# Kernel optimization log

Hardware: AMD Instinct MI355X
Metric: run time of the kernel (lower is better)

## Reference

```python
import jax, jax.numpy as jnp
import numpy as np

POOLED_H, POOLED_W = 7, 7
SPATIAL_SCALE = 0.25
SAMPLING_RATIO = 2
ALIGNED = True

N_IMG, C, H, W = 4, 256, 200, 200
N_ROIS = 1024
IMG_SIZE = H / SPATIAL_SCALE  # 800.0, image-space extent


def setup_inputs() -> dict:
    key = jax.random.key(0)
    k_in, k_b, k_c, k_s = jax.random.split(key, 4)
    inp = jax.random.normal(k_in, (N_IMG, C, H, W), dtype=jnp.float32)
    # Boxes in image coordinates (xyxy), first column = batch index.
    b = jax.random.randint(k_b, (N_ROIS,), 0, N_IMG).astype(jnp.float32)
    ctr = jax.random.uniform(k_c, (N_ROIS, 2), minval=0.0, maxval=IMG_SIZE)
    sz = jax.random.uniform(k_s, (N_ROIS, 2), minval=16.0, maxval=320.0)
    x1 = jnp.clip(ctr[:, 0] - sz[:, 0] * 0.5, 0.0, IMG_SIZE)
    y1 = jnp.clip(ctr[:, 1] - sz[:, 1] * 0.5, 0.0, IMG_SIZE)
    x2 = jnp.clip(ctr[:, 0] + sz[:, 0] * 0.5, 0.0, IMG_SIZE)
    y2 = jnp.clip(ctr[:, 1] + sz[:, 1] * 0.5, 0.0, IMG_SIZE)
    rois = jnp.stack([b, x1, y1, x2, y2], axis=1)
    return {"input": inp, "rois": rois}


def _roi_align(feat_nchw, rois):
    """Faithful port of torchvision.ops.roi_align (avg mode, aligned=True)."""
    n, c, h, w = feat_nchw.shape
    ph, pw, sr = POOLED_H, POOLED_W, SAMPLING_RATIO
    offset = 0.5 if ALIGNED else 0.0

    b_idx = rois[:, 0].astype(jnp.int32)                      # [R]
    x1 = rois[:, 1] * SPATIAL_SCALE - offset
    y1 = rois[:, 2] * SPATIAL_SCALE - offset
    x2 = rois[:, 3] * SPATIAL_SCALE - offset
    y2 = rois[:, 4] * SPATIAL_SCALE - offset
    roi_w, roi_h = x2 - x1, y2 - y1
    if not ALIGNED:
        roi_w = jnp.maximum(roi_w, 1.0)
        roi_h = jnp.maximum(roi_h, 1.0)
    bin_h = roi_h / ph                                        # [R]
    bin_w = roi_w / pw

    # Sample-point grid: per output bin, sr x sr interior points.
    frac = (jnp.arange(sr, dtype=jnp.float32) + 0.5) / sr     # [sr]
    # y coords: [R, ph, sr], x coords: [R, pw, sr]
    ys = y1[:, None, None] + (jnp.arange(ph, dtype=jnp.float32)[None, :, None] + frac[None, None, :]) * bin_h[:, None, None]
    xs = x1[:, None, None] + (jnp.arange(pw, dtype=jnp.float32)[None, :, None] + frac[None, None, :]) * bin_w[:, None, None]
    # Broadcast to full grid [R, ph, pw, sr, sr]
    y = ys[:, :, None, :, None] * jnp.ones((1, 1, pw, 1, sr), jnp.float32)
    x = xs[:, None, :, None, :] * jnp.ones((1, ph, 1, sr, 1), jnp.float32)

    valid = (y >= -1.0) & (y <= h) & (x >= -1.0) & (x <= w)
    yc = jnp.clip(y, 0.0, h - 1)
    xc = jnp.clip(x, 0.0, w - 1)
    y0 = jnp.floor(yc).astype(jnp.int32)
    x0 = jnp.floor(xc).astype(jnp.int32)
    y1i = jnp.minimum(y0 + 1, h - 1)
    x1i = jnp.minimum(x0 + 1, w - 1)
    ly = yc - y0.astype(jnp.float32)
    lx = xc - x0.astype(jnp.float32)
    hy, hx = 1.0 - ly, 1.0 - lx

    feat = jnp.transpose(feat_nchw, (0, 2, 3, 1))             # [N, H, W, C]
    bb = b_idx[:, None, None, None, None]

    def gather(yy, xx):
        return feat[bb, yy, xx]                               # [R, ph, pw, sr, sr, C]

    val = (hy * hx)[..., None] * gather(y0, x0) \
        + (hy * lx)[..., None] * gather(y0, x1i) \
        + (ly * hx)[..., None] * gather(y1i, x0) \
        + (ly * lx)[..., None] * gather(y1i, x1i)
    val = jnp.where(valid[..., None], val, 0.0)
    out = val.mean(axis=(3, 4))                               # avg over sr*sr samples -> [R, ph, pw, C]
    return jnp.transpose(out, (0, 3, 1, 2))                   # [R, C, ph, pw]


def reference(input, rois):
    return _roi_align(input, rois)
```

## Files before the change

### kernel.cpp

```cpp
#include <hip/hip_runtime.h>
#include <hip/hip_bf16.h>


#define CCH 256
#define FH 200
#define FW 200
#define N_ROIS 1024
#define PP 49
#define NG 8
#define GSZ 32
#define PLANE (FH*FW)

__global__ __launch_bounds__(256) void to_grouped(
    const float* __restrict__ in, unsigned short* __restrict__ gout,
    const float* __restrict__ rois, int* __restrict__ perm)
{
    if (blockIdx.x == 0) {
        __shared__ int cnt[4];
        __shared__ int base[4];
        int t = threadIdx.x;
        if (t < 4) cnt[t] = 0;
        __syncthreads();
        int bb[4], po[4];
        #pragma unroll
        for (int r = 0; r < 4; ++r) {
            int ri = r * 256 + t;
            int b = (int)rois[ri * 5];
            bb[r] = b;
            po[r] = atomicAdd(&cnt[b], 1);
        }
        __syncthreads();
        if (t == 0) {
            int s = 0;
            #pragma unroll
            for (int i = 0; i < 4; ++i) { base[i] = s; s += cnt[i]; }
        }
        __syncthreads();
        #pragma unroll
        for (int r = 0; r < 4; ++r)
            perm[base[bb[r]] + po[r]] = r * 256 + t;
    }

    int idx = blockIdx.x * 256 + threadIdx.x;
    int p  = idx % PLANE;
    int bg = idx / PLANE;
    const float* src = in + (size_t)bg * GSZ * PLANE + p;

    unsigned short tmp[GSZ];
    #pragma unroll
    for (int j = 0; j < GSZ; ++j) {
        float f = __builtin_nontemporal_load(&src[(size_t)j * PLANE]);
        unsigned u = __float_as_uint(f);
        tmp[j] = (unsigned short)((u + 0x7FFFu + ((u >> 16) & 1u)) >> 16);
    }
    uint4* dst = (uint4*)(gout + (size_t)idx * GSZ);
    #pragma unroll
    for (int k = 0; k < 4; ++k) {
        uint4 q;
        __builtin_memcpy(&q, &tmp[k * 8], 16);
        dst[k] = q;
    }
}

__device__ __forceinline__ void fma8q(float* acc, uint4 q, float w)
{
    unsigned short u[8];
    __builtin_memcpy(u, &q, 16);
    #pragma unroll
    for (int j = 0; j < 8; ++j)
        acc[j] = fmaf(w, __uint_as_float((unsigned)u[j] << 16), acc[j]);
}

__global__ __launch_bounds__(256) void roi_align_grouped(
    const unsigned short* __restrict__ gfeat,
    const float* __restrict__ rois,
    const int* __restrict__ perm,
    float* __restrict__ out)
{
    int nb  = gridDim.x;
    int vb  = (blockIdx.x & 7) * (nb >> 3) + (blockIdx.x >> 3);
    int idx = vb * 256 + threadIdx.x;

    int s      = idx & 3;
    int bin    = (idx >> 2) % PP;
    int n_slot = (idx / (4 * PP)) % N_ROIS;
    int g      = idx / (4 * PP * N_ROIS);
    int n      = perm[n_slot];
    int ph = bin / 7, pw = bin % 7;

    const float* roi = rois + n * 5;
    int   b  = (int)roi[0];
    float x1 = roi[1] * 0.25f - 0.5f;
    float y1 = roi[2] * 0.25f - 0.5f;
    float x2 = roi[3] * 0.25f - 0.5f;
    float y2 = roi[4] * 0.25f - 0.5f;
    float bin_h = (y2 - y1) / 7.0f;
    float bin_w = (x2 - x1) / 7.0f;

    const unsigned short* plane =
        gfeat + (size_t)(b * NG + g) * (size_t)PLANE * GSZ + s * 8;

    int   yy0[2], yy1[2];
    float wy0[2], wy1[2];
    #pragma unroll
    for (int iy = 0; iy < 2; ++iy) {
        float y = y1 + ((float)ph + ((float)iy + 0.5f) * 0.5f) * bin_h;
        float v = (y >= -1.0f && y <= (float)FH) ? 1.0f : 0.0f;
        float yc = fminf(fmaxf(y, 0.0f), (float)(FH - 1));
        int   y0 = (int)yc;
        yy0[iy] = y0;
        yy1[iy] = min(y0 + 1, FH - 1);
        float ly = yc - (float)y0;
        wy1[iy] = ly * v;
        wy0[iy] = (1.0f - ly) * v;
    }
    int   xx0[2], xx1[2];
    float wx0[2], wx1[2];
    #pragma unroll
    for (int ix = 0; ix < 2; ++ix) {
        float x = x1 + ((float)pw + ((float)ix + 0.5f) * 0.5f) * bin_w;
        float v = (x >= -1.0f && x <= (float)FW) ? 1.0f : 0.0f;
        float xc = fminf(fmaxf(x, 0.0f), (float)(FW - 1));
        int   x0 = (int)xc;
        xx0[ix] = x0;
        xx1[ix] = min(x0 + 1, FW - 1);
        float lx = xc - (float)x0;
        wx1[ix] = lx * v;
        wx0[ix] = (1.0f - lx) * v;
    }

    float acc[8] = {0, 0, 0, 0, 0, 0, 0, 0};

    #pragma unroll
    for (int iy = 0; iy < 2; ++iy) {
        const unsigned short* r0 = plane + (size_t)(yy0[iy] * FW) * GSZ;
        const unsigned short* r1 = plane + (size_t)(yy1[iy] * FW) * GSZ;
        #pragma unroll
        for (int ix = 0; ix < 2; ++ix) {
            uint4 qA = *(const uint4*)(r0 + (size_t)xx0[ix] * GSZ);
            uint4 qB = *(const uint4*)(r0 + (size_t)xx1[ix] * GSZ);
            uint4 qC = *(const uint4*)(r1 + (size_t)xx0[ix] * GSZ);
            uint4 qD = *(const uint4*)(r1 + (size_t)xx1[ix] * GSZ);
            fma8q(acc, qA, wy0[iy] * wx0[ix]);
            fma8q(acc, qB, wy0[iy] * wx1[ix]);
            fma8q(acc, qC, wy1[iy] * wx0[ix]);
            fma8q(acc, qD, wy1[iy] * wx1[ix]);
        }
    }

    float* o = out + ((size_t)n * CCH + g * GSZ + s * 8) * PP + bin;
    #pragma unroll
    for (int j = 0; j < 8; ++j)
        __builtin_nontemporal_store(acc[j] * 0.25f, o + j * PP);
}

__global__ __launch_bounds__(256) void roi_align_fallback(
    const float* __restrict__ feat, const float* __restrict__ rois,
    float* __restrict__ out, int total)
{
    int nb  = gridDim.x;
    int vid = (blockIdx.x & 7) * (nb >> 3) + (blockIdx.x >> 3);
    int idx = vid * 256 + threadIdx.x;
    if (idx >= total) return;
    int pw = idx % 7;
    int ph = (idx / 7) % 7;
    int n  = (idx / 49) & (N_ROIS - 1);
    int c  = idx / (49 * N_ROIS);

    const float* roi = rois + n * 5;
    int   b  = (int)roi[0];
    float x1 = roi[1] * 0.25f - 0.5f;
    float y1 = roi[2] * 0.25f - 0.5f;
    float x2 = roi[3] * 0.25f - 0.5f;
    float y2 = roi[4] * 0.25f - 0.5f;
    float bin_h = (y2 - y1) / 7.0f;
    float bin_w = (x2 - x1) / 7.0f;
    const float* plane = feat + ((size_t)b * CCH + c) * PLANE;

    float acc = 0.0f;
    #pragma unroll
    for (int iy = 0; iy < 2; ++iy) {
        float y = y1 + ((float)ph + ((float)iy + 0.5f) * 0.5f) * bin_h;
        if (y < -1.0f || y > (float)FH) continue;
        float yc = fminf(fmaxf(y, 0.0f), (float)(FH - 1));
        int y0 = (int)yc, y1i = min(y0 + 1, FH - 1);
        float ly = yc - (float)y0, hy = 1.0f - ly;
        #pragma unroll
        for (int ix = 0; ix < 2; ++ix) {
            float x = x1 + ((float)pw + ((float)ix + 0.5f) * 0.5f) * bin_w;
            if (x < -1.0f || x > (float)FW) continue;
            float xc = fminf(fmaxf(x, 0.0f), (float)(FW - 1));
            int x0 = (int)xc, x1i = min(x0 + 1, FW - 1);
            float lx = xc - (float)x0, hx = 1.0f - lx;
            acc += hy * (hx * plane[y0 * FW + x0] + lx * plane[y0 * FW + x1i])
                 + ly * (hx * plane[y1i * FW + x0] + lx * plane[y1i * FW + x1i]);
        }
    }
    out[((size_t)n * CCH + c) * PP + ph * 7 + pw] = acc * 0.25f;
}

extern "C" void kernel_launch(void* const* d_in, const int* in_sizes, int n_in,
                              void* d_out, int out_size, void* d_ws, size_t ws_size,
                              hipStream_t stream)
{
    const float* feat = (const float*)d_in[0];
    const float* rois = (const float*)d_in[1];
    float* out = (float*)d_out;

    const size_t gfeat_bytes = (size_t)4 * NG * PLANE * GSZ * 2;
    const size_t ws_needed = gfeat_bytes + N_ROIS * sizeof(int);

    if (ws_size >= ws_needed) {
        unsigned short* gfeat = (unsigned short*)d_ws;
        int* perm = (int*)((char*)d_ws + gfeat_bytes);
        to_grouped<<<(4 * NG * PLANE) / 256, 256, 0, stream>>>(feat, gfeat, rois, perm);
        int items = NG * N_ROIS * PP * 4;
        roi_align_grouped<<<items / 256, 256, 0, stream>>>(gfeat, rois, perm, out);
    } else {
        int total = out_size;
        int grid = (total + 255) / 256;
        roi_align_fallback<<<grid, 256, 0, stream>>>(feat, rois, out, total);
    }
}
```

Baseline: 296.2 us.

## Fuse regroup and ROI-align into one persistent cooperative kernel with grid sync

Replaces the two-kernel sequence (bf16 channel regrouping, then ROI align) with a single cooperative persistent kernel of 1024 blocks that runs both phases, separated by a grid-wide sync. Each block's XCD-derived index selects the channel group it converts and later reads, so the regrouped data is meant to stay in that XCD's L2. This removes one kernel launch and the inter-kernel gap. In exchange it adds the cost of a grid barrier and a fixed grid-stride schedule. If the cooperative launch fails, it falls back to the old two-kernel path.

```diff
diff --git a/kernel.cpp b/kernel.cpp
--- a/kernel.cpp
+++ b/kernel.cpp
@@ -1,5 +1,6 @@
 #include <hip/hip_runtime.h>
 #include <hip/hip_bf16.h>
+#include <hip/hip_cooperative_groups.h>
 
 
 #define CCH 256
@@ -11,6 +12,152 @@
 #define GSZ 32
 #define PLANE (FH*FW)
 
+namespace cg = cooperative_groups;
+
+__device__ __forceinline__ void fma8q(float* acc, uint4 q, float w)
+{
+    unsigned short u[8];
+    __builtin_memcpy(u, &q, 16);
+    #pragma unroll
+    for (int j = 0; j < 8; ++j)
+        acc[j] = fmaf(w, __uint_as_float((unsigned)u[j] << 16), acc[j]);
+}
+
+__global__ __launch_bounds__(256, 4) void fused_roi_align(
+    const float* __restrict__ in,
+    const float* __restrict__ rois,
+    unsigned short* __restrict__ gfeat,
+    int* __restrict__ perm,
+    float* __restrict__ out)
+{
+    const int t     = threadIdx.x;
+    const int xcd   = blockIdx.x & 7;
+    const int local = blockIdx.x >> 3;
+
+    if (blockIdx.x == 0) {
+        __shared__ int cnt[4];
+        __shared__ int base[4];
+        if (t < 4) cnt[t] = 0;
+        __syncthreads();
+        int bb[4], po[4];
+        #pragma unroll
+        for (int r = 0; r < 4; ++r) {
+            int ri = r * 256 + t;
+            int b = (int)rois[ri * 5];
+            bb[r] = b;
+            po[r] = atomicAdd(&cnt[b], 1);
+        }
+        __syncthreads();
+        if (t == 0) {
+            int s = 0;
+            #pragma unroll
+            for (int i = 0; i < 4; ++i) { base[i] = s; s += cnt[i]; }
+        }
+        __syncthreads();
+        #pragma unroll
+        for (int r = 0; r < 4; ++r)
+            perm[base[bb[r]] + po[r]] = r * 256 + t;
+    }
+
+    for (int i = local * 256 + t; i < 4 * PLANE; i += 128 * 256) {
+        int b  = i / PLANE;
+        int p  = i - b * PLANE;
+        int bg = (b << 3) + xcd;
+        const float* src = in + (size_t)bg * GSZ * PLANE + p;
+
+        unsigned short tmp[GSZ];
+        #pragma unroll
+        for (int j = 0; j < GSZ; ++j) {
+            float f = __builtin_nontemporal_load(&src[(size_t)j * PLANE]);
+            unsigned u = __float_as_uint(f);
+            tmp[j] = (unsigned short)((u + 0x7FFFu + ((u >> 16) & 1u)) >> 16);
+        }
+        uint4* dst = (uint4*)(gfeat + ((size_t)bg * PLANE + p) * GSZ);
+        #pragma unroll
+        for (int k = 0; k < 4; ++k) {
+            uint4 q;
+            __builtin_memcpy(&q, &tmp[k * 8], 16);
+            dst[k] = q;
+        }
+    }
+
+    cg::this_grid().sync();
+
+    const int g = xcd;
+    for (int i = local * 256 + t; i < N_ROIS * PP * 4; i += 128 * 256) {
+        int s      = i & 3;
+        int bin    = (i >> 2) % PP;
+        int n_slot = (i >> 2) / PP;
+        int n      = perm[n_slot];
+        int ph = bin / 7, pw = bin % 7;
+
+        const float* roi = rois + n * 5;
+        int   b  = (int)roi[0];
+        float x1 = roi[1] * 0.25f - 0.5f;
+        float y1 = roi[2] * 0.25f - 0.5f;
+        float x2 = roi[3] * 0.25f - 0.5f;
+        float y2 = roi[4] * 0.25f - 0.5f;
+        float bin_h = (y2 - y1) / 7.0f;
+        float bin_w = (x2 - x1) / 7.0f;
+
+        const unsigned short* plane =
+            gfeat + (size_t)(b * NG + g) * (size_t)PLANE * GSZ + s * 8;
+
+        int   yy0[2], yy1[2];
+        float wy0[2], wy1[2];
+        #pragma unroll
+        for (int iy = 0; iy < 2; ++iy) {
+            float y = y1 + ((float)ph + ((float)iy + 0.5f) * 0.5f) * bin_h;
+            float v = (y >= -1.0f && y <= (float)FH) ? 1.0f : 0.0f;
+            float yc = fminf(fmaxf(y, 0.0f), (float)(FH - 1));
+            int   y0 = (int)yc;
+            yy0[iy] = y0;
+            yy1[iy] = min(y0 + 1, FH - 1);
+            float ly = yc - (float)y0;
+            wy1[iy] = ly * v;
+            wy0[iy] = (1.0f - ly) * v;
+        }
+        int   xx0[2], xx1[2];
+        float wx0[2], wx1[2];
+        #pragma unroll
+        for (int ix = 0; ix < 2; ++ix) {
+            float x = x1 + ((float)pw + ((float)ix + 0.5f) * 0.5f) * bin_w;
+            float v = (x >= -1.0f && x <= (float)FW) ? 1.0f : 0.0f;
+            float xc = fminf(fmaxf(x, 0.0f), (float)(FW - 1));
+            int   x0 = (int)xc;
+            xx0[ix] = x0;
+            xx1[ix] = min(x0 + 1, FW - 1);
+            float lx = xc - (float)x0;
+            wx1[ix] = lx * v;
+            wx0[ix] = (1.0f - lx) * v;
+        }
+
+        float acc[8] = {0, 0, 0, 0, 0, 0, 0, 0};
+
+        #pragma unroll
+        for (int iy = 0; iy < 2; ++iy) {
+            const unsigned short* r0 = plane + (size_t)(yy0[iy] * FW) * GSZ;
+            const unsigned short* r1 = plane + (size_t)(yy1[iy] * FW) * GSZ;
+            #pragma unroll
+            for (int ix = 0; ix < 2; ++ix) {
+                uint4 qA = *(const uint4*)(r0 + (size_t)xx0[ix] * GSZ);
+                uint4 qB = *(const uint4*)(r0 + (size_t)xx1[ix] * GSZ);
+                uint4 qC = *(const uint4*)(r1 + (size_t)xx0[ix] * GSZ);
+                uint4 qD = *(const uint4*)(r1 + (size_t)xx1[ix] * GSZ);
+                fma8q(acc, qA, wy0[iy] * wx0[ix]);
+                fma8q(acc, qB, wy0[iy] * wx1[ix]);
+                fma8q(acc, qC, wy1[iy] * wx0[ix]);
+                fma8q(acc, qD, wy1[iy] * wx1[ix]);
+            }
+        }
+
+        float* o = out + ((size_t)n * CCH + g * GSZ + s * 8) * PP + bin;
+        #pragma unroll
+        for (int j = 0; j < 8; ++j)
+            __builtin_nontemporal_store(acc[j] * 0.25f, o + j * PP);
+    }
+}
+
 __global__ __launch_bounds__(256) void to_grouped(
     const float* __restrict__ in, unsigned short* __restrict__ gout,
     const float* __restrict__ rois, int* __restrict__ perm)
@@ -60,15 +207,6 @@
         __builtin_memcpy(&q, &tmp[k * 8], 16);
         dst[k] = q;
     }
-}
-
-__device__ __forceinline__ void fma8q(float* acc, uint4 q, float w)
-{
-    unsigned short u[8];
-    __builtin_memcpy(u, &q, 16);
-    #pragma unroll
-    for (int j = 0; j < 8; ++j)
-        acc[j] = fmaf(w, __uint_as_float((unsigned)u[j] << 16), acc[j]);
 }
 
 __global__ __launch_bounds__(256) void roi_align_grouped(
@@ -213,9 +351,17 @@
     if (ws_size >= ws_needed) {
         unsigned short* gfeat = (unsigned short*)d_ws;
         int* perm = (int*)((char*)d_ws + gfeat_bytes);
-        to_grouped<<<(4 * NG * PLANE) / 256, 256, 0, stream>>>(feat, gfeat, rois, perm);
-        int items = NG * N_ROIS * PP * 4;
-        roi_align_grouped<<<items / 256, 256, 0, stream>>>(gfeat, rois, perm, out);
+
+        void* args[5] = { (void*)&feat, (void*)&rois, (void*)&gfeat,
+                          (void*)&perm, (void*)&out };
+        hipError_t e = hipLaunchCooperativeKernel(
+            reinterpret_cast<void*>(fused_roi_align),
+            dim3(1024), dim3(256), args, 0, stream);
+        if (e != hipSuccess) {
+            to_grouped<<<(4 * NG * PLANE) / 256, 256, 0, stream>>>(feat, gfeat, rois, perm);
+            int items = NG * N_ROIS * PP * 4;
+            roi_align_grouped<<<items / 256, 256, 0, stream>>>(gfeat, rois, perm, out);
+        }
     } else {
         int total = out_size;
         int grid = (total + 255) / 256;
```

Result: slower. 489.1 us (+65.1%).
